# Optimization experiments

Measured on AMD Instinct MI355X. Metric: run time of the kernel, lower is better.

## Reference

```python
import jax, jax.numpy as jnp
import numpy as np

HIDDEN = 1280
HEADS = 16
HEAD_DIM = HIDDEN // HEADS  # 80
TOTAL = 8192
N_CHUNKS = 8


def rotate_half(x):
    x1, x2 = jnp.split(x, 2, axis=-1)
    return jnp.concatenate([-x2, x1], axis=-1)


def setup_inputs() -> dict:
    key = jax.random.key(0)
    ks = jax.random.split(key, 7)
    hidden_states = jax.random.normal(ks[0], (TOTAL, HIDDEN), dtype=jnp.float32)
    cos = jax.random.uniform(ks[1], (TOTAL, HEAD_DIM), dtype=jnp.float32)
    sin = jax.random.uniform(ks[2], (TOTAL, HEAD_DIM), dtype=jnp.float32)
    s = 1.0 / np.sqrt(HIDDEN)
    w_qkv = jax.random.normal(ks[3], (HIDDEN, 3 * HIDDEN), dtype=jnp.float32) * s
    b_qkv = jax.random.normal(ks[4], (3 * HIDDEN,), dtype=jnp.float32) * 0.01
    w_proj = jax.random.normal(ks[5], (HIDDEN, HIDDEN), dtype=jnp.float32) * s
    b_proj = jax.random.normal(ks[6], (HIDDEN,), dtype=jnp.float32) * 0.01
    return {"hidden_states": hidden_states, "cos": cos, "sin": sin,
            "w_qkv": w_qkv, "b_qkv": b_qkv, "w_proj": w_proj,
            "b_proj": b_proj, "n_chunks": N_CHUNKS}


def reference(hidden_states, cos, sin, w_qkv, b_qkv, w_proj, b_proj, n_chunks):
    T, D = hidden_states.shape
    C = int(n_chunks)
    L = T // C  # equal-length chunks (block-diagonal varlen attention)
    H, hd = HEADS, HEAD_DIM
    scale = hd ** -0.5

    qkv = hidden_states @ w_qkv + b_qkv                    # [T, 3D]
    q, k, v = jnp.split(qkv, 3, axis=-1)
    # [C, L, H, hd]
    q = q.reshape(C, L, H, hd)
    k = k.reshape(C, L, H, hd)
    v = v.reshape(C, L, H, hd)
    cos_c = cos.reshape(C, L, 1, hd)
    sin_c = sin.reshape(C, L, 1, hd)
    q = q * cos_c + rotate_half(q) * sin_c
    k = k * cos_c + rotate_half(k) * sin_c

    # block-diagonal attention: each chunk attends only within itself
    scores = jnp.einsum('clhd,cmhd->chlm', q, k) * scale   # [C, H, L, L]
    weights = jax.nn.softmax(scores.astype(jnp.float32), axis=-1).astype(v.dtype)
    attn = jnp.einsum('chlm,cmhd->clhd', weights, v)       # [C, L, H, hd]
    attn = attn.reshape(T, D)
    return attn @ w_proj + b_proj
```

## Files before the change

kernel.cpp:

```cpp
#include <hip/hip_runtime.h>

#define T_TOK 8192
#define D_HID 1280
#define H_    16
#define HD_   80
#define C_    8
#define L_    1024
#define N3_   3840
#define QPAD  96

typedef _Float16 f16;
typedef __attribute__((ext_vector_type(8))) _Float16 h8;
typedef __attribute__((ext_vector_type(4))) float f32x4;

__global__ __launch_bounds__(256) void convert_x(const float* __restrict__ x,
                                                 f16* __restrict__ y) {
  const int g = blockIdx.x * 256 + threadIdx.x;
  const float4 v = ((const float4*)x)[g];
  f16 o[4] = {(f16)v.x, (f16)v.y, (f16)v.z, (f16)v.w};
  ((uint2*)y)[g] = *(const uint2*)o;
}

__global__ __launch_bounds__(256) void convert_w_t(const float* __restrict__ W,
                                                   f16* __restrict__ Wt,
                                                   int K, int N) {
  __shared__ float tile[32][33];
  const int n0 = blockIdx.x * 32, k0 = blockIdx.y * 32;
  const int c = threadIdx.x & 31, r0 = threadIdx.x >> 5;
#pragma unroll
  for (int it = 0; it < 4; ++it) {
    const int r = r0 + it * 8;
    tile[r][c] = W[(size_t)(k0 + r) * N + n0 + c];
  }
  __syncthreads();
#pragma unroll
  for (int it = 0; it < 4; ++it) {
    const int r = r0 + it * 8;
    Wt[(size_t)(n0 + r) * K + k0 + c] = (f16)tile[c][r];
  }
}

__device__ __forceinline__ void stage_tile(const f16* __restrict__ gbase, int K,
                                           f16* sdst, int wave, int lane) {
#pragma unroll
  for (int rnd = 0; rnd < 2; ++rnd) {
    const int idx = rnd * 256 + wave * 64 + lane;
    const int row = idx >> 2;
    const int part = (idx & 3) ^ ((row >> 1) & 3);
    const f16* gp = gbase + (size_t)row * K + part * 8;
    __builtin_amdgcn_global_load_lds(
        (const __attribute__((address_space(1))) void*)gp,
        (__attribute__((address_space(3))) void*)(sdst + (rnd * 256 + wave * 64) * 8),
        16, 0, 0);
  }
}

__device__ __forceinline__ h8 fragld(const f16* s, int row, int quad) {
  const int pp = quad ^ ((row >> 1) & 3);
  return *(const h8*)&s[row * 32 + pp * 8];
}

__global__ __launch_bounds__(256) void gemm_f16(
    const f16* __restrict__ A, const f16* __restrict__ B,
    const float* __restrict__ bias,
    float* __restrict__ Cf, f16* __restrict__ Ch,
    int M, int N, int K) {
  __shared__ f16 sA[128 * 32], sB[128 * 32];
  const int tid = threadIdx.x;
  const int wave = tid >> 6, lane = tid & 63;
  const int quad = lane >> 4, ln = lane & 15;
  const int bm = blockIdx.y * 128, bn = blockIdx.x * 128;
  const int wm = (wave >> 1) * 64, wn = (wave & 1) * 64;

  f32x4 acc[4][4];
#pragma unroll
  for (int i = 0; i < 4; ++i)
#pragma unroll
    for (int j = 0; j < 4; ++j) acc[i][j] = (f32x4){0.f, 0.f, 0.f, 0.f};

  for (int k0 = 0; k0 < K; k0 += 32) {
    __syncthreads();
    stage_tile(A + (size_t)bm * K + k0, K, sA, wave, lane);
    stage_tile(B + (size_t)bn * K + k0, K, sB, wave, lane);
    __syncthreads();

    h8 af[4], bf[4];
#pragma unroll
    for (int i = 0; i < 4; ++i) af[i] = fragld(sA, wm + i * 16 + ln, quad);
#pragma unroll
    for (int j = 0; j < 4; ++j) bf[j] = fragld(sB, wn + j * 16 + ln, quad);
#pragma unroll
    for (int i = 0; i < 4; ++i)
#pragma unroll
      for (int j = 0; j < 4; ++j)
        acc[i][j] = __builtin_amdgcn_mfma_f32_16x16x32_f16(af[i], bf[j], acc[i][j], 0, 0, 0);
  }

  float bv[4];
#pragma unroll
  for (int j = 0; j < 4; ++j) bv[j] = bias[bn + wn + j * 16 + ln];
#pragma unroll
  for (int i = 0; i < 4; ++i)
#pragma unroll
    for (int j = 0; j < 4; ++j)
#pragma unroll
      for (int r = 0; r < 4; ++r) {
        const int row = bm + wm + i * 16 + quad * 4 + r;
        const int col = bn + wn + j * 16 + ln;
        const float val = acc[i][j][r] + bv[j];
        if (Ch) Ch[(size_t)row * N + col] = (f16)val;
        else    Cf[(size_t)row * N + col] = val;
      }
}

__global__ __launch_bounds__(256) void rope_convert(
    const f16* __restrict__ qkv, const float* __restrict__ cosb,
    const float* __restrict__ sinb, f16* __restrict__ Qb, f16* __restrict__ Kb) {
  const int t = blockIdx.x;
  const int tid = threadIdx.x;
  const size_t rowb = (size_t)t * N3_;
  const float scale = 0.11180339887498949f;
#pragma unroll
  for (int u = 0; u < 10; ++u) {
    const int e = tid + u * 256;
    const int d = e % HD_;
    const bool lo = d < 40;
    const float v = (float)qkv[rowb + e];
    const float p = (float)qkv[rowb + (lo ? e + 40 : e - 40)];
    const float cs = cosb[(size_t)t * HD_ + d];
    const float sn = sinb[(size_t)t * HD_ + d];
    const float o = v * cs + (lo ? -p : p) * sn;
    const int h = (e % D_HID) / HD_;
    const size_t off = ((size_t)h * T_TOK + t) * QPAD + d;
    if (e < D_HID) Qb[off] = (f16)(o * scale);
    else           Kb[off] = (f16)o;
  }
  if (tid < 64) {
    const int qk = tid >> 5, h = (tid >> 1) & 15, half = tid & 1;
    f16* dst = (qk ? Kb : Qb) + ((size_t)h * T_TOK + t) * QPAD + 80 + half * 8;
    const int4 z = make_int4(0, 0, 0, 0);
    *(int4*)dst = z;
  }
}

__global__ __launch_bounds__(256) void vt_convert(const f16* __restrict__ qkv,
                                                  f16* __restrict__ Vt) {
  __shared__ f16 tl[HD_][136];
  const int h = blockIdx.x & 15;
  const int t0 = (blockIdx.x >> 4) * 128;
  const int tid = threadIdx.x;
#pragma unroll
  for (int it = 0; it < 5; ++it) {
    const int e = tid + it * 256;
    const int t = e / 10, pc = e % 10;
    int4 v = *(const int4*)(qkv + (size_t)(t0 + t) * N3_ + 2 * D_HID + h * HD_ + pc * 8);
    f16 tmp[8];
    *(int4*)tmp = v;
#pragma unroll
    for (int u = 0; u < 8; ++u) tl[pc * 8 + u][t] = tmp[u];
  }
  __syncthreads();
#pragma unroll
  for (int it = 0; it < 5; ++it) {
    const int e = tid + it * 256;
    const int d = e >> 4, pt = e & 15;
    *(int4*)(Vt + ((size_t)h * HD_ + d) * T_TOK + t0 + pt * 8) = *(const int4*)&tl[d][pt * 8];
  }
}

__global__ __launch_bounds__(256, 2) void attn_flash(
    const f16* __restrict__ Qb, const f16* __restrict__ Kb,
    const f16* __restrict__ Vt, f16* __restrict__ Oa) {
  __shared__ f16 Ps[4][64][72];
  const int tid = threadIdx.x;
  const int wave = tid >> 6, lane = tid & 63;
  const int quad = lane >> 4, ln = lane & 15;
  const int h = blockIdx.x & 15;
  const int qb = (blockIdx.x >> 4) & 3;
  const int c = blockIdx.x >> 6;
  const int t0 = c * L_ + qb * 256 + wave * 64;
  const size_t hb = (size_t)h * T_TOK;

  h8 aq[4][3];
#pragma unroll
  for (int i = 0; i < 4; ++i)
#pragma unroll
    for (int ks = 0; ks < 3; ++ks)
      aq[i][ks] = *(const h8*)(Qb + (hb + t0 + i * 16 + ln) * QPAD + ks * 32 + quad * 8);

  f32x4 o[4][5];
  float lsum[4][4];
#pragma unroll
  for (int i = 0; i < 4; ++i) {
#pragma unroll
    for (int jn = 0; jn < 5; ++jn) o[i][jn] = (f32x4){0.f, 0.f, 0.f, 0.f};
#pragma unroll
    for (int r = 0; r < 4; ++r) lsum[i][r] = 0.f;
  }

  for (int kb = 0; kb < 16; ++kb) {
    const int kt0 = c * L_ + kb * 64;
#pragma unroll
    for (int j = 0; j < 4; ++j) {
      h8 bk[3];
#pragma unroll
      for (int ks = 0; ks < 3; ++ks)
        bk[ks] = *(const h8*)(Kb + (hb + kt0 + j * 16 + ln) * QPAD + ks * 32 + quad * 8);
      f32x4 s[4];
#pragma unroll
      for (int i = 0; i < 4; ++i) s[i] = (f32x4){0.f, 0.f, 0.f, 0.f};
#pragma unroll
      for (int ks = 0; ks < 3; ++ks)
#pragma unroll
        for (int i = 0; i < 4; ++i)
          s[i] = __builtin_amdgcn_mfma_f32_16x16x32_f16(aq[i][ks], bk[ks], s[i], 0, 0, 0);
#pragma unroll
      for (int i = 0; i < 4; ++i)
#pragma unroll
        for (int r = 0; r < 4; ++r) {
          const float p = __expf(s[i][r]);
          lsum[i][r] += p;
          Ps[wave][i * 16 + quad * 4 + r][j * 16 + ln] = (f16)p;
        }
    }
#pragma unroll
    for (int ks = 0; ks < 2; ++ks) {
      h8 ap[4];
#pragma unroll
      for (int i = 0; i < 4; ++i)
        ap[i] = *(const h8*)&Ps[wave][i * 16 + ln][ks * 32 + quad * 8];
#pragma unroll
      for (int jn = 0; jn < 5; ++jn) {
        const h8 bv = *(const h8*)(Vt + ((size_t)h * HD_ + jn * 16 + ln) * T_TOK
                                   + kt0 + ks * 32 + quad * 8);
#pragma unroll
        for (int i = 0; i < 4; ++i)
          o[i][jn] = __builtin_amdgcn_mfma_f32_16x16x32_f16(ap[i], bv, o[i][jn], 0, 0, 0);
      }
    }
  }

#pragma unroll
  for (int i = 0; i < 4; ++i)
#pragma unroll
    for (int r = 0; r < 4; ++r) {
      float s = lsum[i][r];
#pragma unroll
      for (int off = 1; off < 16; off <<= 1) s += __shfl_xor(s, off);
      lsum[i][r] = 1.f / s;
    }

#pragma unroll
  for (int i = 0; i < 4; ++i)
#pragma unroll
    for (int r = 0; r < 4; ++r) {
      const int t = t0 + i * 16 + quad * 4 + r;
      const float inv = lsum[i][r];
#pragma unroll
      for (int jn = 0; jn < 5; ++jn)
        Oa[(size_t)t * D_HID + h * HD_ + jn * 16 + ln] = (f16)(o[i][jn][r] * inv);
    }
}

extern "C" void kernel_launch(void* const* d_in, const int* in_sizes, int n_in,
                              void* d_out, int out_size, void* d_ws, size_t ws_size,
                              hipStream_t stream) {
  (void)in_sizes; (void)n_in; (void)out_size; (void)ws_size;
  const float* x      = (const float*)d_in[0];
  const float* cosb   = (const float*)d_in[1];
  const float* sinb   = (const float*)d_in[2];
  const float* w_qkv  = (const float*)d_in[3];
  const float* b_qkv  = (const float*)d_in[4];
  const float* w_proj = (const float*)d_in[5];
  const float* b_proj = (const float*)d_in[6];
  float* out = (float*)d_out;

  char* ws = (char*)d_ws;
  f16* qkv_h  = (f16*)(ws);
  f16* attn_h = (f16*)(ws);
  f16* x_h    = (f16*)(ws + 62914560);
  f16* Qb     = (f16*)(ws + 62914560);
  f16* Kb     = (f16*)(ws + 88080384);
  f16* Vt     = (f16*)(ws + 113246208);
  f16* wq_t   = (f16*)(ws + 134217728);
  f16* wp_t   = (f16*)(ws + 144048128);

  convert_x<<<(T_TOK * D_HID / 4) / 256, 256, 0, stream>>>(x, x_h);
  convert_w_t<<<dim3(N3_ / 32, D_HID / 32), 256, 0, stream>>>(w_qkv, wq_t, D_HID, N3_);
  convert_w_t<<<dim3(D_HID / 32, D_HID / 32), 256, 0, stream>>>(w_proj, wp_t, D_HID, D_HID);
  gemm_f16<<<dim3(N3_ / 128, T_TOK / 128), 256, 0, stream>>>(
      x_h, wq_t, b_qkv, nullptr, qkv_h, T_TOK, N3_, D_HID);
  rope_convert<<<T_TOK, 256, 0, stream>>>(qkv_h, cosb, sinb, Qb, Kb);
  vt_convert<<<H_ * (T_TOK / 128), 256, 0, stream>>>(qkv_h, Vt);
  attn_flash<<<C_ * 4 * H_, 256, 0, stream>>>(Qb, Kb, Vt, attn_h);
  gemm_f16<<<dim3(D_HID / 128, T_TOK / 128), 256, 0, stream>>>(
      attn_h, wp_t, b_proj, out, nullptr, T_TOK, D_HID, D_HID);
}
```

Before: 432.4 us.

## Load GEMM fragments directly from global memory with register prefetch

The GEMM kernel no longer stages A and B tiles through LDS with barriers. Each wave now loads its MFMA fragments straight from global memory and prefetches the next K-step into registers while the current step's MFMAs run. This removes the LDS traffic and the two __syncthreads per iteration. In exchange, each block reads the A and B tiles from global memory twice, once per wave sharing them, and per-lane 16-byte strided loads rely on the cache for reuse.

After: 669.2 us. 1.55x slower.

```diff
diff --git a/kernel.cpp b/kernel.cpp
--- a/kernel.cpp
+++ b/kernel.cpp
@@ -40,61 +40,55 @@
   }
 }
 
-__device__ __forceinline__ void stage_tile(const f16* __restrict__ gbase, int K,
-                                           f16* sdst, int wave, int lane) {
-#pragma unroll
-  for (int rnd = 0; rnd < 2; ++rnd) {
-    const int idx = rnd * 256 + wave * 64 + lane;
-    const int row = idx >> 2;
-    const int part = (idx & 3) ^ ((row >> 1) & 3);
-    const f16* gp = gbase + (size_t)row * K + part * 8;
-    __builtin_amdgcn_global_load_lds(
-        (const __attribute__((address_space(1))) void*)gp,
-        (__attribute__((address_space(3))) void*)(sdst + (rnd * 256 + wave * 64) * 8),
-        16, 0, 0);
-  }
-}
-
-__device__ __forceinline__ h8 fragld(const f16* s, int row, int quad) {
-  const int pp = quad ^ ((row >> 1) & 3);
-  return *(const h8*)&s[row * 32 + pp * 8];
-}
-
 __global__ __launch_bounds__(256) void gemm_f16(
     const f16* __restrict__ A, const f16* __restrict__ B,
     const float* __restrict__ bias,
     float* __restrict__ Cf, f16* __restrict__ Ch,
     int M, int N, int K) {
-  __shared__ f16 sA[128 * 32], sB[128 * 32];
   const int tid = threadIdx.x;
   const int wave = tid >> 6, lane = tid & 63;
   const int quad = lane >> 4, ln = lane & 15;
   const int bm = blockIdx.y * 128, bn = blockIdx.x * 128;
   const int wm = (wave >> 1) * 64, wn = (wave & 1) * 64;
 
+  const f16* Ap = A + (size_t)(bm + wm + ln) * K + quad * 8;
+  const f16* Bp = B + (size_t)(bn + wn + ln) * K + quad * 8;
+  const size_t r16 = (size_t)16 * K;
+
   f32x4 acc[4][4];
 #pragma unroll
   for (int i = 0; i < 4; ++i)
 #pragma unroll
     for (int j = 0; j < 4; ++j) acc[i][j] = (f32x4){0.f, 0.f, 0.f, 0.f};
 
-  for (int k0 = 0; k0 < K; k0 += 32) {
-    __syncthreads();
-    stage_tile(A + (size_t)bm * K + k0, K, sA, wave, lane);
-    stage_tile(B + (size_t)bn * K + k0, K, sB, wave, lane);
-    __syncthreads();
-
-    h8 af[4], bf[4];
-#pragma unroll
-    for (int i = 0; i < 4; ++i) af[i] = fragld(sA, wm + i * 16 + ln, quad);
-#pragma unroll
-    for (int j = 0; j < 4; ++j) bf[j] = fragld(sB, wn + j * 16 + ln, quad);
+  h8 af[4], bf[4];
+#pragma unroll
+  for (int i = 0; i < 4; ++i) af[i] = *(const h8*)(Ap + i * r16);
+#pragma unroll
+  for (int j = 0; j < 4; ++j) bf[j] = *(const h8*)(Bp + j * r16);
+
+#pragma unroll 2
+  for (int k0 = 32; k0 < K; k0 += 32) {
+    h8 afn[4], bfn[4];
+#pragma unroll
+    for (int i = 0; i < 4; ++i) afn[i] = *(const h8*)(Ap + i * r16 + k0);
+#pragma unroll
+    for (int j = 0; j < 4; ++j) bfn[j] = *(const h8*)(Bp + j * r16 + k0);
 #pragma unroll
     for (int i = 0; i < 4; ++i)
 #pragma unroll
       for (int j = 0; j < 4; ++j)
         acc[i][j] = __builtin_amdgcn_mfma_f32_16x16x32_f16(af[i], bf[j], acc[i][j], 0, 0, 0);
-  }
+#pragma unroll
+    for (int i = 0; i < 4; ++i) af[i] = afn[i];
+#pragma unroll
+    for (int j = 0; j < 4; ++j) bf[j] = bfn[j];
+  }
+#pragma unroll
+  for (int i = 0; i < 4; ++i)
+#pragma unroll
+    for (int j = 0; j < 4; ++j)
+      acc[i][j] = __builtin_amdgcn_mfma_f32_16x16x32_f16(af[i], bf[j], acc[i][j], 0, 0, 0);
 
   float bv[4];
 #pragma unroll
```
